# Performance work log

Hardware: AMD Instinct MI355X
Metric: run time of the kernel (lower is better)

The kernel has to match this reference:

```python
import jax, jax.numpy as jnp
import numpy as np
import math

B, H, N, D = 2, 16, 2048, 128
SM_SCALE = 1.0 / math.sqrt(D)


def setup_inputs() -> dict:
    key = jax.random.key(0)
    kq, kk, kv = jax.random.split(key, 3)
    q = jax.random.normal(kq, (B, H, N, D), dtype=jnp.float32)
    k = jax.random.normal(kk, (B, H, N, D), dtype=jnp.float32)
    v = jax.random.normal(kv, (B, H, N, D), dtype=jnp.float32)
    return {"q": q, "k": k, "v": v}


def reference(q, k, v):
    # RBF-kernel causal attention (non-softmax):
    #   logits_ij = -sm_scale * ||q_i - k_j||^2
    #            = 2*sm_scale*q_i.k_j - sm_scale*||q_i||^2 - sm_scale*||k_j||^2
    #   p = exp(logits) with causal mask (p_ij = 0 for j > i); out = p @ v
    sm_scale = jnp.float32(SM_SCALE)
    q_sq = sm_scale * jnp.sum(q * q, axis=-1)  # [B,H,N]
    k_sq = sm_scale * jnp.sum(k * k, axis=-1)  # [B,H,N]
    qk = jnp.einsum("bhmd,bhnd->bhmn", q, k)
    logits = (2.0 * sm_scale) * qk - q_sq[..., :, None] - k_sq[..., None, :]
    n = q.shape[2]
    causal = jnp.tril(jnp.ones((n, n), dtype=bool))
    logits = jnp.where(causal, logits, -jnp.inf)
    p = jnp.exp(logits)  # NOT normalized (non-softmax attention)
    out = jnp.einsum("bhmn,bhnd->bhmd", p, v)
    return out
```

## Files before the change

### kernel.cpp

```cpp
#include <hip/hip_runtime.h>
#include <math.h>


#define NSEQ 2048
#define DH   128
#define BHC  32
#define SM_SCALE 0.08838834764831845f

typedef __attribute__((ext_vector_type(8))) short    short8;
typedef __attribute__((ext_vector_type(8))) _Float16 half8;
typedef __attribute__((ext_vector_type(4))) short    short4_;
typedef __attribute__((ext_vector_type(4))) float    float4_;
typedef __attribute__((ext_vector_type(4))) unsigned uint4_;
typedef __attribute__((ext_vector_type(2))) unsigned uint2_;

__device__ __forceinline__ short f2bf(float x){
  union{float f; unsigned u;} a; a.f=x;
  unsigned r = a.u + 0x7fffu + ((a.u>>16)&1u);
  return (short)(r>>16);
}
__device__ __forceinline__ float bf2f(short h){
  union{float f; unsigned u;} a; a.u=((unsigned)(unsigned short)h)<<16; return a.f;
}
__device__ __forceinline__ unsigned packbf(float a, float b){
  return (unsigned)(unsigned short)f2bf(a) | ((unsigned)(unsigned short)f2bf(b)<<16);
}
__device__ __forceinline__ unsigned cvtpk_bf16(float a, float b){
  unsigned r;
  asm("v_cvt_pk_bf16_f32 %0, %1, %2" : "=v"(r) : "v"(a), "v"(b));
  return r;
}

__device__ __forceinline__ void qswap32(unsigned A, unsigned B, unsigned &X, unsigned &Y){
  uint2_ r = __builtin_amdgcn_permlane32_swap(A, B, false, false);
  X = r[0]; Y = r[1];
}
__device__ __forceinline__ void qswap16(unsigned A, unsigned B, unsigned &X, unsigned &Y, int oddq){
#if __has_builtin(__builtin_amdgcn_permlane16_swap)
  uint2_ r = __builtin_amdgcn_permlane16_swap(A, B, false, false);
  X = r[0]; Y = r[1];
#else
  unsigned As = (unsigned)__builtin_amdgcn_ds_swizzle((int)A, 0x401F);
  unsigned Bs = (unsigned)__builtin_amdgcn_ds_swizzle((int)B, 0x401F);
  X = oddq ? Bs : A;
  Y = oddq ? B  : As;
#endif
}

__global__ __launch_bounds__(256)
void prep_kv5(const float* __restrict__ kg, const float* __restrict__ vg,
              _Float16* __restrict__ khg, short* __restrict__ vtg,
              float* __restrict__ ksqg){
  __shared__ unsigned Vls[128*33];
  const int b = blockIdx.x, t = threadIdx.x;
  const int l = t & 63, wv = t >> 6;
  if(b < 1024){
    const int bh = b>>5, jt = b&31;
    const float4_* vb4 = (const float4_*)(vg + ((size_t)bh*NSEQ + (size_t)jt*64)*DH);
    #pragma unroll
    for(int i=0;i<8;++i){
      float4_ own = vb4[i*256 + t];
      float4_ par;
      par.x = __shfl_xor(own.x, 32); par.y = __shfl_xor(own.y, 32);
      par.z = __shfl_xor(own.z, 32); par.w = __shfl_xor(own.w, 32);
      const int hi = (l>>5)&1;
      unsigned w0 = hi ? packbf(par.z, own.z) : packbf(own.x, par.x);
      unsigned w1 = hi ? packbf(par.w, own.w) : packbf(own.y, par.y);
      const int dd = 4*(t&31) + 2*hi;
      const int j2 = 4*i + wv;
      Vls[dd*33 + j2]     = w0;
      Vls[(dd+1)*33 + j2] = w1;
    }
    __syncthreads();
    short* outp = vtg + ((size_t)(bh*32 + jt)*DH)*64;
    #pragma unroll
    for(int it=0; it<4; ++it){
      int idx = t + 256*it;
      int d = idx>>3, slot = idx&7;
      uint4_ o;
      o.x = Vls[d*33 + 4*slot];   o.y = Vls[d*33 + 4*slot+1];
      o.z = Vls[d*33 + 4*slot+2]; o.w = Vls[d*33 + 4*slot+3];
      *(uint4_*)(outp + d*64 + 8*slot) = o;
    }
  } else {
    const int kb = b - 1024;
    const float4_* kb4 = (const float4_*)(kg + (size_t)kb*64*DH);
    #pragma unroll
    for(int i=0;i<8;++i){
      float4_ x = kb4[i*256 + t];
      const int row = 64*kb + 8*i + (t>>5);
      const int d   = 4*(t&31);
      union{ _Float16 h[4]; uint2_ u; } pk;
      pk.h[0]=(_Float16)x.x; pk.h[1]=(_Float16)x.y;
      pk.h[2]=(_Float16)x.z; pk.h[3]=(_Float16)x.w;
      *(uint2_*)(khg + (size_t)row*DH + d) = pk.u;
      float ss = x.x*x.x + x.y*x.y + x.z*x.z + x.w*x.w;
      ss += __shfl_xor(ss,1);  ss += __shfl_xor(ss,2);
      ss += __shfl_xor(ss,4);  ss += __shfl_xor(ss,8);
      ss += __shfl_xor(ss,16);
      if((l&31)==0) ksqg[row] = SM_SCALE*ss;
    }
  }
}

__global__ __launch_bounds__(256,2)
void rbf_attn13(const float* __restrict__ qg,
                const _Float16* __restrict__ khg,
                const short* __restrict__ vtg,
                const float* __restrict__ ksqg,
                float* __restrict__ og){
  __shared__ short Kst[64*128];
  __shared__ short Vst[128*64];
  __shared__ float ksLs[2304];

  const int tid=threadIdx.x;
  const int w=tid>>6, l=tid&63;
  const int quad=l>>4, lr=l&15;
  const int bh=blockIdx.x;
  const int mq = 31 - blockIdx.y;
  const int qbase = 64*mq + 16*w;

  const float*    Qg = qg   + (size_t)bh*NSEQ*DH;
  const _Float16* Kh = khg  + (size_t)bh*NSEQ*DH;
  const short*    Vt = vtg  + (size_t)bh*32*DH*64;
  const float*    Ks = ksqg + (size_t)bh*NSEQ;
  float*          Og = og   + (size_t)bh*NSEQ*DH;

  half8 qf[4];
  float qsq;
  {
    const int qrow = qbase + lr;
    const float* qp = Qg + (size_t)qrow*DH + 8*quad;
    float ss=0.f;
    #pragma unroll
    for(int ks=0;ks<4;++ks){
      float4_ a = *(const float4_*)(qp + 32*ks);
      float4_ b = *(const float4_*)(qp + 32*ks + 4);
      half8 h;
      #pragma unroll
      for(int j=0;j<4;++j){
        h[j]   = (_Float16)a[j];
        h[j+4] = (_Float16)b[j];
        ss += a[j]*a[j] + b[j]*b[j];
      }
      qf[ks]=h;
    }
    ss += __shfl_xor(ss,16);
    ss += __shfl_xor(ss,32);
    qsq = SM_SCALE*ss;
  }

  float4_ oacc[8];
  #pragma unroll
  for(int b2=0;b2<8;++b2) oacc[b2] = (float4_)0.f;

  uint4_ kreg[4], vreg[4];
  float  kqreg = 0.f;
  {
    #pragma unroll
    for(int it=0;it<4;++it){
      int idx = tid + 256*it;
      int row = idx>>4, c = idx&15;
      kreg[it] = *(const uint4_*)(Kh + (size_t)row*DH + 8*c);
      int d = idx>>3, slot = idx&7;
      vreg[it] = *(const uint4_*)(Vt + (size_t)d*64 + 8*slot);
    }
    if(tid<64) kqreg = Ks[tid];
  }

  for(int jt=0; jt<=mq; ++jt){
    #pragma unroll
    for(int it=0;it<4;++it){
      int idx = tid + 256*it;
      int row = idx>>4, c = idx&15;
      *(uint4_*)&Kst[row*128 + 8*(c ^ (row&7))] = kreg[it];
      int d = idx>>3, slot = idx&7;
      *(uint4_*)&Vst[d*64 + 8*(slot ^ (d&7))] = vreg[it];
    }
    if(tid<64) ksLs[tid] = kqreg;
    __syncthreads();

    if(jt < mq){
      const int jc2 = (jt+1)*64;
      #pragma unroll
      for(int it=0;it<4;++it){
        int idx = tid + 256*it;
        int row = idx>>4, c = idx&15;
        kreg[it] = *(const uint4_*)(Kh + (size_t)(jc2+row)*DH + 8*c);
        int d = idx>>3, slot = idx&7;
        vreg[it] = *(const uint4_*)(Vt + ((size_t)(jt+1)*DH + d)*64 + 8*slot);
      }
      if(tid<64) kqreg = Ks[jc2 + tid];
    }

    const bool diag = (jt == mq);
    const int ctmax = diag ? w : 3;
    const int nks2  = (diag && w < 2) ? 1 : 2;

    float4_ sacc[4];
    #pragma unroll
    for(int ct=0;ct<4;++ct) sacc[ct] = (float4_)0.f;

    __builtin_amdgcn_s_setprio(1);
    #pragma unroll
    for(int ks=0;ks<4;++ks){
      half8 kf[4];
      #pragma unroll
      for(int ct=0;ct<4;++ct)
        if(ct<=ctmax)
          kf[ct] = *(const half8*)&Kst[(16*ct+lr)*128 + 8*((4*ks+quad) ^ (lr&7))];
      #pragma unroll
      for(int ct=0;ct<4;++ct)
        if(ct<=ctmax) sacc[ct]=__builtin_amdgcn_mfma_f32_16x16x32_f16(kf[ct],qf[ks],sacc[ct],0,0,0);
    }
    __builtin_amdgcn_s_setprio(0);

    unsigned pk[4][2];
    {
      const int jg0 = 64*jt;
      const int qrow = qbase + lr;
      #pragma unroll
      for(int ct=0;ct<4;++ct){
        if(ct < 2*nks2){
          float4_ kq = *(const float4_*)&ksLs[16*ct + 4*quad];
          const int j0 = jg0 + 16*ct + 4*quad;
          float p[4];
          #pragma unroll
          for(int r=0;r<4;++r){
            float logit = (2.f*SM_SCALE)*sacc[ct][r] - qsq - kq[r];
            p[r] = (j0 + r <= qrow) ? __expf(logit) : 0.f;
          }
          pk[ct][0] = cvtpk_bf16(p[0], p[1]);
          pk[ct][1] = cvtpk_bf16(p[2], p[3]);
        }
      }
    }

    __builtin_amdgcn_s_setprio(1);
    #pragma unroll
    for(int ks2=0;ks2<2;++ks2){
      if(ks2 < nks2){
        unsigned A0,B0,A1,B1;
        qswap32(pk[2*ks2][0], pk[2*ks2+1][0], A0, B0);
        qswap32(pk[2*ks2][1], pk[2*ks2+1][1], A1, B1);
        unsigned w0,w1,w2,w3;
        qswap16(A0, B0, w0, w2, quad&1);
        qswap16(A1, B1, w1, w3, quad&1);
        union{ uint4_ u; short8 s; } pfu;
        pfu.u.x=w0; pfu.u.y=w1; pfu.u.z=w2; pfu.u.w=w3;
        const short8 pf = pfu.s;
        #pragma unroll
        for(int ctv=0;ctv<8;++ctv){
          const short8 vf = *(const short8*)&Vst[(16*ctv+lr)*64 + 8*((4*ks2+quad) ^ (lr&7))];
          oacc[ctv]=__builtin_amdgcn_mfma_f32_16x16x32_bf16(pf,vf,oacc[ctv],0,0,0);
        }
      }
    }
    __builtin_amdgcn_s_setprio(0);

    __syncthreads();
  }

  #pragma unroll
  for(int ctv=0;ctv<8;++ctv)
    #pragma unroll
    for(int r=0;r<4;++r){
      const int qrow = qbase + 4*quad + r;
      Og[(size_t)qrow*DH + 16*ctv + lr] = oacc[ctv][r];
    }
}

#define KSTf 136
#define VSTf 36
#define PSTf 72

__global__ __launch_bounds__(256,2)
void rbf_attn_mfma(const float* __restrict__ qg, const float* __restrict__ kg,
                   const float* __restrict__ vg, float* __restrict__ og){
  __shared__ short    Khi[64*KSTf];
  __shared__ short    Klo[64*KSTf];
  __shared__ unsigned VP [128*VSTf];
  __shared__ short    Pfb[64*PSTf];
  __shared__ float    qsq_s[64];
  __shared__ float    ksq_s[64];

  const int tid=threadIdx.x;
  const int w=tid>>6, l=tid&63;
  const int wr=w>>1, wc=w&1;
  const int quad=l>>4, lr=l&15;
  const int bh=blockIdx.x, yp=blockIdx.y;

  const float* Qg = qg + (size_t)bh*NSEQ*DH;
  const float* Kg = kg + (size_t)bh*NSEQ*DH;
  const float* Vg = vg + (size_t)bh*NSEQ*DH;
  float*       Og = og + (size_t)bh*NSEQ*DH;

  for(int pass=0;pass<2;++pass){
    const int m = pass ? (31-yp) : yp;
    __syncthreads();
    short8 qhf[2][4], qlf[2][4];
    #pragma unroll
    for(int rt=0;rt<2;++rt){
      const int grow = m*64 + 32*wr + 16*rt + lr;
      const float* qp = Qg + (size_t)grow*DH + 8*quad;
      float ss=0.f;
      #pragma unroll
      for(int ks=0;ks<4;++ks){
        float4_ a = *(const float4_*)(qp + 32*ks);
        float4_ b = *(const float4_*)(qp + 32*ks + 4);
        short8 hi, lo;
        #pragma unroll
        for(int j=0;j<4;++j){
          float fa=a[j], fb=b[j];
          short ha=f2bf(fa); hi[j]=ha;   lo[j]=f2bf(fa-bf2f(ha));
          short hb=f2bf(fb); hi[j+4]=hb; lo[j+4]=f2bf(fb-bf2f(hb));
          ss += fa*fa + fb*fb;
        }
        qhf[rt][ks]=hi; qlf[rt][ks]=lo;
      }
      ss += __shfl_xor(ss,16);
      ss += __shfl_xor(ss,32);
      if(wc==0 && quad==0) qsq_s[32*wr+16*rt+lr] = SM_SCALE*ss;
    }
    float4_ oacc[2][4];
    #pragma unroll
    for(int a=0;a<2;++a)
      #pragma unroll
      for(int b=0;b<4;++b) oacc[a][b] = (float4_)0.f;

    const int ntiles = m+1;
    for(int jt=0;jt<ntiles;++jt){
      const int jc = jt*64;
      __syncthreads();
      #pragma unroll
      for(int it=0;it<4;++it){
        const int i = tid + 256*it;
        const int row = i>>4, c0 = 8*(i&15);
        const float* kp = Kg + (size_t)(jc+row)*DH + c0;
        float4_ a = *(const float4_*)kp;
        float4_ b = *(const float4_*)(kp+4);
        short8 hi, lo;
        float ss=0.f;
        #pragma unroll
        for(int j=0;j<4;++j){
          float fa=a[j], fb=b[j];
          short ha=f2bf(fa); hi[j]=ha;   lo[j]=f2bf(fa-bf2f(ha));
          short hb=f2bf(fb); hi[j+4]=hb; lo[j+4]=f2bf(fb-bf2f(hb));
          ss += fa*fa + fb*fb;
        }
        ss += __shfl_xor(ss,1); ss += __shfl_xor(ss,2);
        ss += __shfl_xor(ss,4); ss += __shfl_xor(ss,8);
        if(lr==0) ksq_s[row] = SM_SCALE*ss;
        *(short8*)&Khi[row*KSTf + c0] = hi;
        *(short8*)&Klo[row*KSTf + c0] = lo;
      }
      #pragma unroll
      for(int it=0;it<4;++it){
        const int u = tid + 256*it;
        const int d = u & 127, jg = u >> 7;
        const float* vp = Vg + (size_t)(jc + 8*jg)*DH + d;
        float vv[8];
        #pragma unroll
        for(int jj=0;jj<8;++jj) vv[jj] = vp[(size_t)jj*DH];
        uint4_ pk;
        #pragma unroll
        for(int p2=0;p2<4;++p2)
          pk[p2] = (unsigned)(unsigned short)f2bf(vv[2*p2]) |
                   ((unsigned)(unsigned short)f2bf(vv[2*p2+1])<<16);
        *(uint4_*)&VP[d*VSTf + 4*jg] = pk;
      }
      __syncthreads();
      float4_ sacc[2][2];
      #pragma unroll
      for(int a=0;a<2;++a)
        #pragma unroll
        for(int b=0;b<2;++b) sacc[a][b] = (float4_)0.f;
      #pragma unroll
      for(int ks=0;ks<4;++ks){
        short8 khf[2], klf[2];
        #pragma unroll
        for(int ct=0;ct<2;++ct){
          const int off = (32*wc + 16*ct + lr)*KSTf + 32*ks + 8*quad;
          khf[ct] = *(const short8*)&Khi[off];
          klf[ct] = *(const short8*)&Klo[off];
        }
        #pragma unroll
        for(int rt=0;rt<2;++rt)
          #pragma unroll
          for(int ct=0;ct<2;++ct){
            sacc[rt][ct]=__builtin_amdgcn_mfma_f32_16x16x32_bf16(qhf[rt][ks],khf[ct],sacc[rt][ct],0,0,0);
            sacc[rt][ct]=__builtin_amdgcn_mfma_f32_16x16x32_bf16(qhf[rt][ks],klf[ct],sacc[rt][ct],0,0,0);
            sacc[rt][ct]=__builtin_amdgcn_mfma_f32_16x16x32_bf16(qlf[rt][ks],khf[ct],sacc[rt][ct],0,0,0);
          }
      }
      #pragma unroll
      for(int rt=0;rt<2;++rt){
        float qs[4];
        #pragma unroll
        for(int r=0;r<4;++r) qs[r]=qsq_s[32*wr+16*rt+4*quad+r];
        #pragma unroll
        for(int ct=0;ct<2;++ct){
          const float ksq = ksq_s[32*wc+16*ct+lr];
          const int colg = jc + 32*wc+16*ct+lr;
          #pragma unroll
          for(int r=0;r<4;++r){
            const int rowg = m*64 + 32*wr+16*rt+4*quad+r;
            float logit = (2.f*SM_SCALE)*sacc[rt][ct][r] - qs[r] - ksq;
            float p = (colg<=rowg)? __expf(logit) : 0.f;
            Pfb[(32*wr+16*rt+4*quad+r)*PSTf + 32*wc+16*ct+lr] = f2bf(p);
          }
        }
      }
      __syncthreads();
      #pragma unroll
      for(int ks2=0;ks2<2;++ks2){
        short8 pf[2];
        #pragma unroll
        for(int rt=0;rt<2;++rt)
          pf[rt] = *(const short8*)&Pfb[(32*wr+16*rt+lr)*PSTf + 32*ks2 + 8*quad];
        #pragma unroll
        for(int ctv=0;ctv<4;++ctv){
          const int d = 64*wc + 16*ctv + lr;
          const short8 vfb = *(const short8*)((const short*)VP + d*(2*VSTf) + 32*ks2 + 8*quad);
          #pragma unroll
          for(int rt=0;rt<2;++rt)
            oacc[rt][ctv]=__builtin_amdgcn_mfma_f32_16x16x32_bf16(pf[rt],vfb,oacc[rt][ctv],0,0,0);
        }
      }
    }
    #pragma unroll
    for(int rt=0;rt<2;++rt)
      #pragma unroll
      for(int ctv=0;ctv<4;++ctv)
        #pragma unroll
        for(int r=0;r<4;++r){
          const int rowg = m*64 + 32*wr + 16*rt + 4*quad + r;
          Og[(size_t)rowg*DH + 64*wc + 16*ctv + lr] = oacc[rt][ctv][r];
        }
  }
}

extern "C" void kernel_launch(void* const* d_in, const int* in_sizes, int n_in,
                              void* d_out, int out_size, void* d_ws, size_t ws_size,
                              hipStream_t stream) {
  const float* q = (const float*)d_in[0];
  const float* k = (const float*)d_in[1];
  const float* v = (const float*)d_in[2];
  float* out = (float*)d_out;

  const size_t nElem = (size_t)BHC*NSEQ*DH;
  const size_t need  = nElem*2*sizeof(short) + (size_t)BHC*NSEQ*sizeof(float);

  if(ws_size >= need){
    _Float16* khg = (_Float16*)d_ws;
    short*    vtg = (short*)(khg + nElem);
    float*    ksqg = (float*)(vtg + nElem);
    prep_kv5<<<2048, 256, 0, stream>>>(k, v, khg, vtg, ksqg);
    rbf_attn13<<<dim3(BHC,32), 256, 0, stream>>>(q, khg, vtg, ksqg, out);
  } else {
    rbf_attn_mfma<<<dim3(BHC,16), 256, 0, stream>>>(q, k, v, out);
  }
}
```

Before: 193.1 us.

## Double-buffer K/V tiles in LDS and pair causal query blocks per workgroup

Each workgroup now processes two query tiles (31-y and y), so every block does the same amount of causal work and the grid shrinks from 32 to 16 blocks per head. K/V tiles are double-buffered in shared memory, which leaves one barrier per iteration instead of two, and the next tile is written to the spare buffer after the compute step. This aims to remove load imbalance across the causal triangle and cut barrier stalls. The cost is twice the LDS per block, which may lower occupancy, and fewer blocks in the grid (512) to spread across the CUs.

```diff
diff --git a/kernel.cpp b/kernel.cpp
--- a/kernel.cpp
+++ b/kernel.cpp
@@ -104,21 +104,20 @@
 }
 
 __global__ __launch_bounds__(256,2)
-void rbf_attn13(const float* __restrict__ qg,
+void rbf_attn14(const float* __restrict__ qg,
                 const _Float16* __restrict__ khg,
                 const short* __restrict__ vtg,
                 const float* __restrict__ ksqg,
                 float* __restrict__ og){
-  __shared__ short Kst[64*128];
-  __shared__ short Vst[128*64];
-  __shared__ float ksLs[2304];
+  __shared__ short Kst[2][64*128];
+  __shared__ short Vst[2][128*64];
+  __shared__ float ksLs[2][64];
 
   const int tid=threadIdx.x;
   const int w=tid>>6, l=tid&63;
   const int quad=l>>4, lr=l&15;
   const int bh=blockIdx.x;
-  const int mq = 31 - blockIdx.y;
-  const int qbase = 64*mq + 16*w;
+  const int y=blockIdx.y;
 
   const float*    Qg = qg   + (size_t)bh*NSEQ*DH;
   const _Float16* Kh = khg  + (size_t)bh*NSEQ*DH;
@@ -126,148 +125,170 @@
   const float*    Ks = ksqg + (size_t)bh*NSEQ;
   float*          Og = og   + (size_t)bh*NSEQ*DH;
 
-  half8 qf[4];
-  float qsq;
-  {
-    const int qrow = qbase + lr;
-    const float* qp = Qg + (size_t)qrow*DH + 8*quad;
-    float ss=0.f;
-    #pragma unroll
-    for(int ks=0;ks<4;++ks){
-      float4_ a = *(const float4_*)(qp + 32*ks);
-      float4_ b = *(const float4_*)(qp + 32*ks + 4);
-      half8 h;
-      #pragma unroll
-      for(int j=0;j<4;++j){
-        h[j]   = (_Float16)a[j];
-        h[j+4] = (_Float16)b[j];
-        ss += a[j]*a[j] + b[j]*b[j];
-      }
-      qf[ks]=h;
-    }
-    ss += __shfl_xor(ss,16);
-    ss += __shfl_xor(ss,32);
-    qsq = SM_SCALE*ss;
-  }
-
-  float4_ oacc[8];
-  #pragma unroll
-  for(int b2=0;b2<8;++b2) oacc[b2] = (float4_)0.f;
-
-  uint4_ kreg[4], vreg[4];
-  float  kqreg = 0.f;
-  {
-    #pragma unroll
-    for(int it=0;it<4;++it){
-      int idx = tid + 256*it;
-      int row = idx>>4, c = idx&15;
-      kreg[it] = *(const uint4_*)(Kh + (size_t)row*DH + 8*c);
-      int d = idx>>3, slot = idx&7;
-      vreg[it] = *(const uint4_*)(Vt + (size_t)d*64 + 8*slot);
-    }
-    if(tid<64) kqreg = Ks[tid];
-  }
-
-  for(int jt=0; jt<=mq; ++jt){
-    #pragma unroll
-    for(int it=0;it<4;++it){
-      int idx = tid + 256*it;
-      int row = idx>>4, c = idx&15;
-      *(uint4_*)&Kst[row*128 + 8*(c ^ (row&7))] = kreg[it];
-      int d = idx>>3, slot = idx&7;
-      *(uint4_*)&Vst[d*64 + 8*(slot ^ (d&7))] = vreg[it];
-    }
-    if(tid<64) ksLs[tid] = kqreg;
-    __syncthreads();
-
-    if(jt < mq){
-      const int jc2 = (jt+1)*64;
+  #pragma unroll 1
+  for(int phase=0; phase<2; ++phase){
+    const int mq = phase ? y : (31 - y);
+    const int qbase = 64*mq + 16*w;
+
+    half8 qf[4];
+    float qsq;
+    {
+      const int qrow = qbase + lr;
+      const float* qp = Qg + (size_t)qrow*DH + 8*quad;
+      float ss=0.f;
+      #pragma unroll
+      for(int ks=0;ks<4;++ks){
+        float4_ a = *(const float4_*)(qp + 32*ks);
+        float4_ b = *(const float4_*)(qp + 32*ks + 4);
+        half8 h;
+        #pragma unroll
+        for(int j=0;j<4;++j){
+          h[j]   = (_Float16)a[j];
+          h[j+4] = (_Float16)b[j];
+          ss += a[j]*a[j] + b[j]*b[j];
+        }
+        qf[ks]=h;
+      }
+      ss += __shfl_xor(ss,16);
+      ss += __shfl_xor(ss,32);
+      qsq = SM_SCALE*ss;
+    }
+
+    float4_ oacc[8];
+    #pragma unroll
+    for(int b2=0;b2<8;++b2) oacc[b2] = (float4_)0.f;
+
+    uint4_ kreg[4], vreg[4];
+    float  kqreg = 0.f;
+    {
       #pragma unroll
       for(int it=0;it<4;++it){
         int idx = tid + 256*it;
         int row = idx>>4, c = idx&15;
-        kreg[it] = *(const uint4_*)(Kh + (size_t)(jc2+row)*DH + 8*c);
+        kreg[it] = *(const uint4_*)(Kh + (size_t)row*DH + 8*c);
         int d = idx>>3, slot = idx&7;
-        vreg[it] = *(const uint4_*)(Vt + ((size_t)(jt+1)*DH + d)*64 + 8*slot);
-      }
-      if(tid<64) kqreg = Ks[jc2 + tid];
-    }
-
-    const bool diag = (jt == mq);
-    const int ctmax = diag ? w : 3;
-    const int nks2  = (diag && w < 2) ? 1 : 2;
-
-    float4_ sacc[4];
-    #pragma unroll
-    for(int ct=0;ct<4;++ct) sacc[ct] = (float4_)0.f;
-
-    __builtin_amdgcn_s_setprio(1);
-    #pragma unroll
-    for(int ks=0;ks<4;++ks){
-      half8 kf[4];
-      #pragma unroll
-      for(int ct=0;ct<4;++ct)
-        if(ct<=ctmax)
-          kf[ct] = *(const half8*)&Kst[(16*ct+lr)*128 + 8*((4*ks+quad) ^ (lr&7))];
-      #pragma unroll
-      for(int ct=0;ct<4;++ct)
-        if(ct<=ctmax) sacc[ct]=__builtin_amdgcn_mfma_f32_16x16x32_f16(kf[ct],qf[ks],sacc[ct],0,0,0);
-    }
-    __builtin_amdgcn_s_setprio(0);
-
-    unsigned pk[4][2];
+        vreg[it] = *(const uint4_*)(Vt + (size_t)d*64 + 8*slot);
+      }
+      if(tid<64) kqreg = Ks[tid];
+    }
+    __syncthreads();
     {
-      const int jg0 = 64*jt;
-      const int qrow = qbase + lr;
-      #pragma unroll
-      for(int ct=0;ct<4;++ct){
-        if(ct < 2*nks2){
-          float4_ kq = *(const float4_*)&ksLs[16*ct + 4*quad];
-          const int j0 = jg0 + 16*ct + 4*quad;
-          float p[4];
+      #pragma unroll
+      for(int it=0;it<4;++it){
+        int idx = tid + 256*it;
+        int row = idx>>4, c = idx&15;
+        *(uint4_*)&Kst[0][row*128 + 8*(c ^ (row&7))] = kreg[it];
+        int d = idx>>3, slot = idx&7;
+        *(uint4_*)&Vst[0][d*64 + 8*(slot ^ (d&7))] = vreg[it];
+      }
+      if(tid<64) ksLs[0][tid] = kqreg;
+    }
+
+    int cur = 0;
+    for(int jt=0; jt<=mq; ++jt){
+      __syncthreads();
+
+      if(jt < mq){
+        const int jc2 = (jt+1)*64;
+        #pragma unroll
+        for(int it=0;it<4;++it){
+          int idx = tid + 256*it;
+          int row = idx>>4, c = idx&15;
+          kreg[it] = *(const uint4_*)(Kh + (size_t)(jc2+row)*DH + 8*c);
+          int d = idx>>3, slot = idx&7;
+          vreg[it] = *(const uint4_*)(Vt + ((size_t)(jt+1)*DH + d)*64 + 8*slot);
+        }
+        if(tid<64) kqreg = Ks[jc2 + tid];
+      }
+
+      const bool diag = (jt == mq);
+      const int ctmax = diag ? w : 3;
+      const int nks2  = (diag && w < 2) ? 1 : 2;
+
+      float4_ sacc[4];
+      #pragma unroll
+      for(int ct=0;ct<4;++ct) sacc[ct] = (float4_)0.f;
+
+      __builtin_amdgcn_s_setprio(1);
+      #pragma unroll
+      for(int ks=0;ks<4;++ks){
+        half8 kf[4];
+        #pragma unroll
+        for(int ct=0;ct<4;++ct)
+          if(ct<=ctmax)
+            kf[ct] = *(const half8*)&Kst[cur][(16*ct+lr)*128 + 8*((4*ks+quad) ^ (lr&7))];
+        #pragma unroll
+        for(int ct=0;ct<4;++ct)
+          if(ct<=ctmax) sacc[ct]=__builtin_amdgcn_mfma_f32_16x16x32_f16(kf[ct],qf[ks],sacc[ct],0,0,0);
+      }
+      __builtin_amdgcn_s_setprio(0);
+
+      unsigned pk[4][2];
+      {
+        const int jg0 = 64*jt;
+        const int qrow = qbase + lr;
+        #pragma unroll
+        for(int ct=0;ct<4;++ct){
+          if(ct < 2*nks2){
+            float4_ kq = *(const float4_*)&ksLs[cur][16*ct + 4*quad];
+            const int j0 = jg0 + 16*ct + 4*quad;
+            float p[4];
+            #pragma unroll
+            for(int r=0;r<4;++r){
+              float logit = (2.f*SM_SCALE)*sacc[ct][r] - qsq - kq[r];
+              p[r] = (j0 + r <= qrow) ? __expf(logit) : 0.f;
+            }
+            pk[ct][0] = cvtpk_bf16(p[0], p[1]);
+            pk[ct][1] = cvtpk_bf16(p[2], p[3]);
+          }
+        }
+      }
+
+      __builtin_amdgcn_s_setprio(1);
+      #pragma unroll
+      for(int ks2=0;ks2<2;++ks2){
+        if(ks2 < nks2){
+          unsigned A0,B0,A1,B1;
+          qswap32(pk[2*ks2][0], pk[2*ks2+1][0], A0, B0);
+          qswap32(pk[2*ks2][1], pk[2*ks2+1][1], A1, B1);
+          unsigned w0,w1,w2,w3;
+          qswap16(A0, B0, w0, w2, quad&1);
+          qswap16(A1, B1, w1, w3, quad&1);
+          union{ uint4_ u; short8 s; } pfu;
+          pfu.u.x=w0; pfu.u.y=w1; pfu.u.z=w2; pfu.u.w=w3;
+          const short8 pf = pfu.s;
           #pragma unroll
-          for(int r=0;r<4;++r){
-            float logit = (2.f*SM_SCALE)*sacc[ct][r] - qsq - kq[r];
-            p[r] = (j0 + r <= qrow) ? __expf(logit) : 0.f;
+          for(int ctv=0;ctv<8;++ctv){
+            const short8 vf = *(const short8*)&Vst[cur][(16*ctv+lr)*64 + 8*((4*ks2+quad) ^ (lr&7))];
+            oacc[ctv]=__builtin_amdgcn_mfma_f32_16x16x32_bf16(pf,vf,oacc[ctv],0,0,0);
           }
-          pk[ct][0] = cvtpk_bf16(p[0], p[1]);
-          pk[ct][1] = cvtpk_bf16(p[2], p[3]);
-        }
-      }
-    }
-
-    __builtin_amdgcn_s_setprio(1);
-    #pragma unroll
-    for(int ks2=0;ks2<2;++ks2){
-      if(ks2 < nks2){
-        unsigned A0,B0,A1,B1;
-        qswap32(pk[2*ks2][0], pk[2*ks2+1][0], A0, B0);
-        qswap32(pk[2*ks2][1], pk[2*ks2+1][1], A1, B1);
-        unsigned w0,w1,w2,w3;
-        qswap16(A0, B0, w0, w2, quad&1);
-        qswap16(A1, B1, w1, w3, quad&1);
-        union{ uint4_ u; short8 s; } pfu;
-        pfu.u.x=w0; pfu.u.y=w1; pfu.u.z=w2; pfu.u.w=w3;
-        const short8 pf = pfu.s;
-        #pragma unroll
-        for(int ctv=0;ctv<8;++ctv){
-          const short8 vf = *(const short8*)&Vst[(16*ctv+lr)*64 + 8*((4*ks2+quad) ^ (lr&7))];
-          oacc[ctv]=__builtin_amdgcn_mfma_f32_16x16x32_bf16(pf,vf,oacc[ctv],0,0,0);
-        }
-      }
-    }
-    __builtin_amdgcn_s_setprio(0);
-
-    __syncthreads();
+        }
+      }
+      __builtin_amdgcn_s_setprio(0);
+
+      if(jt < mq){
+        const int nxt = cur^1;
+        #pragma unroll
+        for(int it=0;it<4;++it){
+          int idx = tid + 256*it;
+          int row = idx>>4, c = idx&15;
+          *(uint4_*)&Kst[nxt][row*128 + 8*(c ^ (row&7))] = kreg[it];
+          int d = idx>>3, slot = idx&7;
+          *(uint4_*)&Vst[nxt][d*64 + 8*(slot ^ (d&7))] = vreg[it];
+        }
+        if(tid<64) ksLs[nxt][tid] = kqreg;
+      }
+      cur ^= 1;
+    }
+
+    #pragma unroll
+    for(int ctv=0;ctv<8;++ctv)
+      #pragma unroll
+      for(int r=0;r<4;++r){
+        const int qrow = qbase + 4*quad + r;
+        Og[(size_t)qrow*DH + 16*ctv + lr] = oacc[ctv][r];
+      }
   }
-
-  #pragma unroll
-  for(int ctv=0;ctv<8;++ctv)
-    #pragma unroll
-    for(int r=0;r<4;++r){
-      const int qrow = qbase + 4*quad + r;
-      Og[(size_t)qrow*DH + 16*ctv + lr] = oacc[ctv][r];
-    }
 }
 
 #define KSTf 136
@@ -456,7 +477,7 @@
     short*    vtg = (short*)(khg + nElem);
     float*    ksqg = (float*)(vtg + nElem);
     prep_kv5<<<2048, 256, 0, stream>>>(k, v, khg, vtg, ksqg);
-    rbf_attn13<<<dim3(BHC,32), 256, 0, stream>>>(q, khg, vtg, ksqg, out);
+    rbf_attn14<<<dim3(BHC,16), 256, 0, stream>>>(q, khg, vtg, ksqg, out);
   } else {
     rbf_attn_mfma<<<dim3(BHC,16), 256, 0, stream>>>(q, k, v, out);
   }
```

Result: no change. 191.5 us (-0.8%).
